# Kernel optimization log

Measured on AMD Instinct MI355X. Metric: run time of the kernel, lower is better.

The kernel has to match this reference:

```python
import jax, jax.numpy as jnp
import numpy as np

BATCH = 2048
N = 2 * BATCH
TEMP = 0.5
BN_EPS = 1e-5
COS_EPS = 1e-8

# Precompute (constant) flat indices of the negative entries: all (i,j) with
# j != i and j != i +- BATCH. Each row has exactly N-2 negatives.
_mask = np.ones((N, N), dtype=bool)
np.fill_diagonal(_mask, False)
for _i in range(BATCH):
    _mask[_i, BATCH + _i] = False
    _mask[BATCH + _i, _i] = False
NEG_IDX = np.nonzero(_mask.reshape(-1))[0]  # (N*(N-2),)


def _projector(h, W1, gamma, beta, W2, b2):
    # Linear (no bias) -> BatchNorm1d (training-mode batch stats) -> ReLU -> Linear
    x = h @ W1.T                                   # (B, latent)
    mu = jnp.mean(x, axis=0)
    var = jnp.mean(jnp.square(x - mu), axis=0)     # biased var, as torch BN
    x = (x - mu) * jax.lax.rsqrt(var + BN_EPS) * gamma + beta
    x = jax.nn.relu(x)
    return x @ W2.T + b2                           # (B, proj)


def setup_inputs() -> dict:
    key = jax.random.key(0)
    ks = jax.random.split(key, 4)
    latent, proj = 2048, 256
    return {
        "h_i": jax.random.normal(ks[0], (BATCH, latent), jnp.float32),
        "h_j": jax.random.normal(ks[1], (BATCH, latent), jnp.float32),
        "W1": jax.random.normal(ks[2], (latent, latent), jnp.float32) / np.sqrt(latent),
        "gamma": jnp.ones((latent,), jnp.float32),
        "beta": jnp.zeros((latent,), jnp.float32),
        "W2": jax.random.normal(ks[3], (proj, latent), jnp.float32) / np.sqrt(latent),
        "b2": jnp.zeros((proj,), jnp.float32),
    }


def reference(h_i, h_j, W1, gamma, beta, W2, b2):
    z_i = _projector(h_i, W1, gamma, beta, W2, b2)
    z_j = _projector(h_j, W1, gamma, beta, W2, b2)
    z = jnp.concatenate([z_i, z_j], axis=0)                      # (N, proj)
    # cosine similarity: normalize once, then a single GEMM
    zn = z / jnp.maximum(jnp.linalg.norm(z, axis=1, keepdims=True), COS_EPS)
    sim = (zn @ zn.T) / TEMP                                     # (N, N)
    sim_i_j = jnp.diagonal(sim, offset=BATCH)                    # (BATCH,)
    sim_j_i = jnp.diagonal(sim, offset=-BATCH)                   # (BATCH,)
    positives = jnp.concatenate([sim_i_j, sim_j_i])[:, None]     # (N, 1)
    negatives = sim.reshape(-1)[NEG_IDX].reshape(N, N - 2)       # (N, N-2)
    logits = jnp.concatenate([positives, negatives], axis=1)     # (N, N-1)
    # cross-entropy with label 0 for every row, reduction='sum', then / N
    loss = jnp.sum(jax.nn.logsumexp(logits, axis=1) - logits[:, 0]) / N
    return loss
```

## Files before the change

### kernel.cpp

```cpp
#include <hip/hip_runtime.h>
#include <hip/hip_fp8.h>
#include <math.h>

#define BATCH   2048
#define NROWS   4096
#define LATENT  2048
#define PROJ    256
#define BN_EPS  1e-5f
#define COS_EPS 1e-8f
#define W1SCALE 32.0f
#define W1INV   (1.0f / 32.0f)
#define ZNSCALE 16.0f
#define SIMSCALE (1.0f / 128.0f)

typedef float f32x4 __attribute__((ext_vector_type(4)));
typedef long  i64;

__device__ __forceinline__ unsigned short f2bf(float f) {
    union { float f; unsigned int u; } c; c.f = f;
    return (unsigned short)((c.u + 0x7FFFu + ((c.u >> 16) & 1u)) >> 16);
}
__device__ __forceinline__ float bf2f(unsigned short h) {
    union { unsigned int u; float f; } c; c.u = ((unsigned int)h) << 16;
    return c.f;
}
__device__ __forceinline__ unsigned char f2fp8(float f) {
    __hip_fp8_e4m3 t(f);
    return (unsigned char)t.__x;
}
__device__ __forceinline__ float fp82f(unsigned char b) {
    __hip_fp8_e4m3 t; t.__x = b;
    return (float)t;
}

__device__ __forceinline__ void gl_lds16(const void* g, void* l) {
    __builtin_amdgcn_global_load_lds(
        (const __attribute__((address_space(1))) void*)g,
        (__attribute__((address_space(3))) void*)l, 16, 0, 0);
}

__device__ __forceinline__ int mix8(int R) {
    return (R & 7) ^ ((R >> 1) & 4);
}

#define G1 1048576
#define G2 2097152
#define G3 3145728
#define G4 3276800
__global__ __launch_bounds__(256) void cvt_all_kernel(
    const float* __restrict__ h_i, const float* __restrict__ h_j,
    const float* __restrict__ W1,  const float* __restrict__ W2,
    unsigned char* __restrict__ Hq, unsigned char* __restrict__ W1q,
    unsigned char* __restrict__ W2q, float* __restrict__ zeroacc)
{
    int i = blockIdx.x * 256 + threadIdx.x;
    if (blockIdx.x == 0) {
        #pragma unroll
        for (int u = 0; u < 48; ++u) zeroacc[u * 256 + threadIdx.x] = 0.f;
    }
    if (i >= G4) return;
    if (i < G2) {
        const float* src = (i < G1) ? h_i : h_j;
        int off = (i < G1) ? i : i - G1;
        float4 v = reinterpret_cast<const float4*>(src)[off];
        uchar4 o;
        o.x = f2fp8(v.x); o.y = f2fp8(v.y); o.z = f2fp8(v.z); o.w = f2fp8(v.w);
        reinterpret_cast<uchar4*>(Hq)[i] = o;
    } else if (i < G3) {
        int off = i - G2;
        float4 v = reinterpret_cast<const float4*>(W1)[off];
        uchar4 o;
        o.x = f2fp8(v.x * W1SCALE); o.y = f2fp8(v.y * W1SCALE);
        o.z = f2fp8(v.z * W1SCALE); o.w = f2fp8(v.w * W1SCALE);
        reinterpret_cast<uchar4*>(W1q)[off] = o;
    } else {
        int off = i - G3;
        float4 v = reinterpret_cast<const float4*>(W2)[off];
        uchar4 o;
        o.x = f2fp8(v.x * W1SCALE); o.y = f2fp8(v.y * W1SCALE);
        o.z = f2fp8(v.z * W1SCALE); o.w = f2fp8(v.w * W1SCALE);
        reinterpret_cast<uchar4*>(W2q)[off] = o;
    }
}

template<int KSTRIDE, int KLEN>
__device__ __forceinline__ void fp8_loop(
    const unsigned char* __restrict__ Ab, const unsigned char* __restrict__ Bb,
    unsigned char* As, unsigned char* Bs, f32x4 acc[4][2], int tid)
{
    const int wid = tid >> 6, lane = tid & 63;
    const int mblk = (wid >> 1) * 64, nblk = (wid & 1) * 32;
    const int lr = lane & 15, lk = lane >> 4;
    for (int k0 = 0; k0 < KLEN; k0 += 128) {
        __syncthreads();
        #pragma unroll
        for (int u = 0; u < 4; ++u) {
            int li = u * 256 + tid;
            int r = li >> 3, s = li & 7;
            gl_lds16(Ab + (size_t)r * KSTRIDE + k0 + ((s ^ mix8(r)) * 16), As + li * 16);
        }
        #pragma unroll
        for (int u = 0; u < 2; ++u) {
            int li = u * 256 + tid;
            int r = li >> 3, s = li & 7;
            gl_lds16(Bb + (size_t)r * KSTRIDE + k0 + ((s ^ mix8(r)) * 16), Bs + li * 16);
        }
        __syncthreads();
        i64 af[4][4], bv[2][4];
        #pragma unroll
        for (int i = 0; i < 4; ++i) {
            int R = mblk + i * 16 + lr;
            int mr = mix8(R);
            int base = R * 128 + (lk & 1) * 8;
            #pragma unroll
            for (int t = 0; t < 4; ++t) {
                int g = 2 * t + (lk >> 1);
                af[i][t] = *reinterpret_cast<const i64*>(As + base + ((g ^ mr) << 4));
            }
        }
        #pragma unroll
        for (int j = 0; j < 2; ++j) {
            int R = nblk + j * 16 + lr;
            int mr = mix8(R);
            int base = R * 128 + (lk & 1) * 8;
            #pragma unroll
            for (int t = 0; t < 4; ++t) {
                int g = 2 * t + (lk >> 1);
                bv[j][t] = *reinterpret_cast<const i64*>(Bs + base + ((g ^ mr) << 4));
            }
        }
        #pragma unroll
        for (int t = 0; t < 4; ++t)
            #pragma unroll
            for (int i = 0; i < 4; ++i)
                #pragma unroll
                for (int j = 0; j < 2; ++j)
                    acc[i][j] = __builtin_amdgcn_mfma_f32_16x16x32_fp8_fp8(
                        af[i][t], bv[j][t], acc[i][j], 0, 0, 0);
    }
}

__global__ __launch_bounds__(256, 4) void gemm1_fp8(
    const unsigned char* __restrict__ Hq, const unsigned char* __restrict__ W1q,
    unsigned char* __restrict__ Xq, float* __restrict__ sums, float* __restrict__ sumsqs)
{
    __shared__ __align__(16) unsigned char As[128 * 128];
    __shared__ __align__(16) unsigned char Bs[64 * 128];
    const int tid = threadIdx.x;
    const int m0 = blockIdx.y * 128, n0 = blockIdx.x * 64;
    f32x4 zero = {0.f, 0.f, 0.f, 0.f};
    f32x4 acc[4][2];
    #pragma unroll
    for (int i = 0; i < 4; ++i) { acc[i][0] = zero; acc[i][1] = zero; }
    fp8_loop<LATENT, LATENT>(Hq + (size_t)m0 * LATENT, W1q + (size_t)n0 * LATENT,
                             As, Bs, acc, tid);
    const int wid = tid >> 6, lane = tid & 63;
    const int mblk = (wid >> 1) * 64, nblk = (wid & 1) * 32;
    const int lr = lane & 15, lq = lane >> 4;
    const int half = m0 >> 11;
    #pragma unroll
    for (int j = 0; j < 2; ++j) {
        float s = 0.f, q = 0.f;
        #pragma unroll
        for (int i = 0; i < 4; ++i)
            #pragma unroll
            for (int r = 0; r < 4; ++r) {
                float v = acc[i][j][r] * W1INV;
                s += v; q += v * v;
                int row = m0 + mblk + i * 16 + lq * 4 + r;
                int col = n0 + nblk + j * 16 + lr;
                Xq[(size_t)row * LATENT + col] = f2fp8(v);
            }
        s += __shfl_xor(s, 16, 64);  q += __shfl_xor(q, 16, 64);
        s += __shfl_xor(s, 32, 64);  q += __shfl_xor(q, 32, 64);
        if (lq == 0) {
            int col = n0 + nblk + j * 16 + lr;
            atomicAdd(&sums[half * LATENT + col], s);
            atomicAdd(&sumsqs[half * LATENT + col], q);
        }
    }
}

__global__ __launch_bounds__(256) void bnrelu8_kernel(
    unsigned char* __restrict__ Xq, const float* __restrict__ sums,
    const float* __restrict__ sumsqs, const float* __restrict__ gamma,
    const float* __restrict__ beta)
{
    const int row = blockIdx.x;
    const int half = row >> 11;
    const int col = threadIdx.x * 8;
    size_t idx = (size_t)row * LATENT + col;
    uchar4 a = *reinterpret_cast<const uchar4*>(Xq + idx);
    uchar4 b = *reinterpret_cast<const uchar4*>(Xq + idx + 4);
    uchar4 oa, ob;
    #pragma unroll
    for (int u = 0; u < 8; ++u) {
        int c = col + u;
        int g = half * LATENT + c;
        float mu  = sums[g] * (1.0f / BATCH);
        float var = sumsqs[g] * (1.0f / BATCH) - mu * mu;
        float sc = gamma[c] * rsqrtf(var + BN_EPS);
        float sh = beta[c] - mu * sc;
        unsigned char x = (u < 4) ? ((const unsigned char*)&a)[u] : ((const unsigned char*)&b)[u - 4];
        unsigned char o = f2fp8(fmaxf(fmaf(fp82f(x), sc, sh), 0.f));
        if (u < 4) ((unsigned char*)&oa)[u] = o; else ((unsigned char*)&ob)[u - 4] = o;
    }
    *reinterpret_cast<uchar4*>(Xq + idx) = oa;
    *reinterpret_cast<uchar4*>(Xq + idx + 4) = ob;
}

__global__ __launch_bounds__(256, 4) void gemm2_fp8(
    const unsigned char* __restrict__ Xq, const unsigned char* __restrict__ W2q,
    unsigned short* __restrict__ Zpb)
{
    __shared__ __align__(16) unsigned char As[128 * 128];
    __shared__ __align__(16) unsigned char Bs[64 * 128];
    const int tid = threadIdx.x;
    const int m0 = blockIdx.y * 128, n0 = blockIdx.x * 64, kc = blockIdx.z;
    f32x4 zero = {0.f, 0.f, 0.f, 0.f};
    f32x4 acc[4][2];
    #pragma unroll
    for (int i = 0; i < 4; ++i) { acc[i][0] = zero; acc[i][1] = zero; }
    fp8_loop<LATENT, 512>(Xq + (size_t)m0 * LATENT + kc * 512,
                          W2q + (size_t)n0 * LATENT + kc * 512, As, Bs, acc, tid);
    unsigned short* Zk = Zpb + (size_t)kc * NROWS * PROJ;
    const int wid = tid >> 6, lane = tid & 63;
    const int mblk = (wid >> 1) * 64, nblk = (wid & 1) * 32;
    const int lr = lane & 15, lq = lane >> 4;
    #pragma unroll
    for (int i = 0; i < 4; ++i)
        #pragma unroll
        for (int j = 0; j < 2; ++j)
            #pragma unroll
            for (int r = 0; r < 4; ++r) {
                int row = m0 + mblk + i * 16 + lq * 4 + r;
                int col = n0 + nblk + j * 16 + lr;
                Zk[(size_t)row * PROJ + col] = f2bf(acc[i][j][r] * W1INV);
            }
}

__global__ __launch_bounds__(256) void rownorm_kernel(
    const unsigned short* __restrict__ Zpb, const float* __restrict__ b2,
    unsigned char* __restrict__ ZNq)
{
    const int wave = threadIdx.x >> 6;
    const int lane = threadIdx.x & 63;
    const int row = blockIdx.x * 4 + wave;
    float v[4];
    float sq = 0.f;
    #pragma unroll
    for (int i = 0; i < 4; ++i) {
        int col = lane + i * 64;
        float t = b2[col];
        #pragma unroll
        for (int c = 0; c < 4; ++c)
            t += bf2f(Zpb[(size_t)c * NROWS * PROJ + (size_t)row * PROJ + col]);
        v[i] = t;
        sq += t * t;
    }
    #pragma unroll
    for (int off = 32; off > 0; off >>= 1) sq += __shfl_xor(sq, off, 64);
    float inv = ZNSCALE / fmaxf(sqrtf(sq), COS_EPS);
    #pragma unroll
    for (int i = 0; i < 4; ++i)
        ZNq[(size_t)row * PROJ + lane + i * 64] = f2fp8(v[i] * inv);
}

__global__ __launch_bounds__(256) void simlse_fp8(
    const unsigned char* __restrict__ ZNq, float* __restrict__ rowsum,
    float* __restrict__ dgA, float* __restrict__ posA)
{
    if (blockIdx.x < blockIdx.y) return;
    __shared__ __align__(16) unsigned char As[128 * 256];
    __shared__ __align__(16) unsigned char Bs[128 * 256];
    const int tid = threadIdx.x;
    const int r0 = blockIdx.y * 128, j0 = blockIdx.x * 128;
    const bool offdiag = (j0 != r0);
    const unsigned char* Ab = ZNq + (size_t)r0 * PROJ;
    const unsigned char* Bb = ZNq + (size_t)j0 * PROJ;
    #pragma unroll
    for (int u = 0; u < 8; ++u) {
        int li = u * 256 + tid;
        int r = li >> 4, s = li & 15;
        int c = s ^ (r & 15);
        gl_lds16(Ab + (size_t)r * PROJ + c * 16, As + li * 16);
    }
    #pragma unroll
    for (int u = 0; u < 8; ++u) {
        int li = u * 256 + tid;
        int r = li >> 4, s = li & 15;
        int c = s ^ (r & 15);
        gl_lds16(Bb + (size_t)r * PROJ + c * 16, Bs + li * 16);
    }
    __syncthreads();
    const int wid = tid >> 6, lane = tid & 63;
    const int mblk = (wid >> 1) * 64, nblk = (wid & 1) * 64;
    const int lr = lane & 15, lk = lane >> 4;
    f32x4 zero = {0.f, 0.f, 0.f, 0.f};
    f32x4 acc[4][4];
    #pragma unroll
    for (int i = 0; i < 4; ++i)
        #pragma unroll
        for (int j = 0; j < 4; ++j) acc[i][j] = zero;
    #pragma unroll
    for (int t = 0; t < 8; ++t) {
        int g = 2 * t + (lk >> 1);
        i64 af[4], bv[4];
        #pragma unroll
        for (int i = 0; i < 4; ++i) {
            int R = mblk + i * 16 + lr;
            af[i] = *reinterpret_cast<const i64*>(As + R * 256 + ((g ^ (R & 15)) << 4) + (lk & 1) * 8);
        }
        #pragma unroll
        for (int j = 0; j < 4; ++j) {
            int R = nblk + j * 16 + lr;
            bv[j] = *reinterpret_cast<const i64*>(Bs + R * 256 + ((g ^ (R & 15)) << 4) + (lk & 1) * 8);
        }
        #pragma unroll
        for (int i = 0; i < 4; ++i)
            #pragma unroll
            for (int j = 0; j < 4; ++j)
                acc[i][j] = __builtin_amdgcn_mfma_f32_16x16x32_fp8_fp8(af[i], bv[j], acc[i][j], 0, 0, 0);
    }
    const int lq = lane >> 4;
    float tcol[4] = {0.f, 0.f, 0.f, 0.f};
    #pragma unroll
    for (int i = 0; i < 4; ++i)
        #pragma unroll
        for (int r = 0; r < 4; ++r) {
            int R = r0 + mblk + i * 16 + lq * 4 + r;
            int P = (R < BATCH) ? R + BATCH : R - BATCH;
            float t = 0.f;
            #pragma unroll
            for (int j = 0; j < 4; ++j) {
                int J = j0 + nblk + j * 16 + lr;
                float s = acc[i][j][r] * SIMSCALE;
                float e = __expf(s);
                t += e;
                tcol[j] += e;
                if (J == R) dgA[R] = e;
                if (J == P) { posA[R] = s; posA[J] = s; }
            }
            t += __shfl_xor(t, 1, 64);
            t += __shfl_xor(t, 2, 64);
            t += __shfl_xor(t, 4, 64);
            t += __shfl_xor(t, 8, 64);
            if (lr == 0) atomicAdd(&rowsum[R], t);
        }
    if (offdiag) {
        #pragma unroll
        for (int j = 0; j < 4; ++j) {
            float c = tcol[j];
            c += __shfl_xor(c, 16, 64);
            c += __shfl_xor(c, 32, 64);
            if (lq == 0) atomicAdd(&rowsum[j0 + nblk + j * 16 + lr], c);
        }
    }
}

__global__ __launch_bounds__(256) void loss_kernel(
    const float* __restrict__ rowsum, const float* __restrict__ dgA,
    const float* __restrict__ posA, float* __restrict__ out)
{
    __shared__ float red[256];
    float s = 0.f;
    for (int r = threadIdx.x; r < NROWS; r += 256)
        s += logf(rowsum[r] - dgA[r]) - posA[r];
    red[threadIdx.x] = s;
    __syncthreads();
    for (int off = 128; off > 0; off >>= 1) {
        if (threadIdx.x < off) red[threadIdx.x] += red[threadIdx.x + off];
        __syncthreads();
    }
    if (threadIdx.x == 0) out[0] = red[0] * (1.0f / NROWS);
}

extern "C" void kernel_launch(void* const* d_in, const int* in_sizes, int n_in,
                              void* d_out, int out_size, void* d_ws, size_t ws_size,
                              hipStream_t stream)
{
    const float* h_i   = (const float*)d_in[0];
    const float* h_j   = (const float*)d_in[1];
    const float* W1    = (const float*)d_in[2];
    const float* gamma = (const float*)d_in[3];
    const float* beta  = (const float*)d_in[4];
    const float* W2    = (const float*)d_in[5];
    const float* b2    = (const float*)d_in[6];
    float* out = (float*)d_out;

    unsigned short* Zpb = (unsigned short*)d_ws;
    float* sums   = (float*)(Zpb + (size_t)4 * NROWS * PROJ);
    float* sumsqs = sums + 2 * LATENT;
    float* rowsum = sumsqs + 2 * LATENT;
    float* dgA    = rowsum + NROWS;
    float* posA   = dgA + NROWS;
    unsigned char* Hq  = (unsigned char*)(posA + NROWS);
    unsigned char* W1q = Hq + (size_t)NROWS * LATENT;
    unsigned char* W2q = W1q + (size_t)LATENT * LATENT;
    unsigned char* Xq  = W2q + (size_t)PROJ * LATENT;
    unsigned char* ZNq = Xq + (size_t)NROWS * LATENT;

    cvt_all_kernel<<<(G4 + 255) / 256, 256, 0, stream>>>(h_i, h_j, W1, W2, Hq, W1q, W2q, sums);
    gemm1_fp8<<<dim3(LATENT / 64, NROWS / 128), 256, 0, stream>>>(Hq, W1q, Xq, sums, sumsqs);
    bnrelu8_kernel<<<NROWS, 256, 0, stream>>>(Xq, sums, sumsqs, gamma, beta);
    gemm2_fp8<<<dim3(PROJ / 64, NROWS / 128, 4), 256, 0, stream>>>(Xq, W2q, Zpb);
    rownorm_kernel<<<NROWS / 4, 256, 0, stream>>>(Zpb, b2, ZNq);
    simlse_fp8<<<dim3(NROWS / 128, NROWS / 128), 256, 0, stream>>>(ZNq, rowsum, dgA, posA);
    loss_kernel<<<1, 256, 0, stream>>>(rowsum, dgA, posA, out);
}
```

Baseline: 173.3 us.

## Fuse second projection GEMM with row normalization into single kernel

Replaces the split-K gemm2 (which wrote four bf16 partial Z buffers) and the separate rownorm kernel with one kernel. Each block computes a full 128x256 output tile over the whole K dimension, adds the bias, reduces squared norms across the two column waves through shared memory, and writes normalized fp8 rows directly. This removes the partial-sum round trip through global memory and one launch. The cost is only 32 blocks for this GEMM, which leaves most CUs idle, plus more accumulator registers per thread (acc[4][8]).

```diff
diff --git a/kernel.cpp b/kernel.cpp
--- a/kernel.cpp
+++ b/kernel.cpp
@@ -16,14 +16,6 @@
 typedef float f32x4 __attribute__((ext_vector_type(4)));
 typedef long  i64;
 
-__device__ __forceinline__ unsigned short f2bf(float f) {
-    union { float f; unsigned int u; } c; c.f = f;
-    return (unsigned short)((c.u + 0x7FFFu + ((c.u >> 16) & 1u)) >> 16);
-}
-__device__ __forceinline__ float bf2f(unsigned short h) {
-    union { unsigned int u; float f; } c; c.u = ((unsigned int)h) << 16;
-    return c.f;
-}
 __device__ __forceinline__ unsigned char f2fp8(float f) {
     __hip_fp8_e4m3 t(f);
     return (unsigned char)t.__x;
@@ -32,13 +24,11 @@
     __hip_fp8_e4m3 t; t.__x = b;
     return (float)t;
 }
-
 __device__ __forceinline__ void gl_lds16(const void* g, void* l) {
     __builtin_amdgcn_global_load_lds(
         (const __attribute__((address_space(1))) void*)g,
         (__attribute__((address_space(3))) void*)l, 16, 0, 0);
 }
-
 __device__ __forceinline__ int mix8(int R) {
     return (R & 7) ^ ((R >> 1) & 4);
 }
@@ -209,61 +199,98 @@
     *reinterpret_cast<uchar4*>(Xq + idx + 4) = ob;
 }
 
-__global__ __launch_bounds__(256, 4) void gemm2_fp8(
+__global__ __launch_bounds__(256) void gemm2rn_fp8(
     const unsigned char* __restrict__ Xq, const unsigned char* __restrict__ W2q,
-    unsigned short* __restrict__ Zpb)
+    const float* __restrict__ b2, unsigned char* __restrict__ ZNq)
 {
     __shared__ __align__(16) unsigned char As[128 * 128];
-    __shared__ __align__(16) unsigned char Bs[64 * 128];
+    __shared__ __align__(16) unsigned char Bs[256 * 128];
+    __shared__ float red[128][2];
     const int tid = threadIdx.x;
-    const int m0 = blockIdx.y * 128, n0 = blockIdx.x * 64, kc = blockIdx.z;
+    const int m0 = blockIdx.x * 128;
+    const unsigned char* Ab = Xq + (size_t)m0 * LATENT;
+    const int wid = tid >> 6, lane = tid & 63;
+    const int mblk = (wid >> 1) * 64, nblk = (wid & 1) * 128;
+    const int lr = lane & 15, lk = lane >> 4;
     f32x4 zero = {0.f, 0.f, 0.f, 0.f};
-    f32x4 acc[4][2];
-    #pragma unroll
-    for (int i = 0; i < 4; ++i) { acc[i][0] = zero; acc[i][1] = zero; }
-    fp8_loop<LATENT, 512>(Xq + (size_t)m0 * LATENT + kc * 512,
-                          W2q + (size_t)n0 * LATENT + kc * 512, As, Bs, acc, tid);
-    unsigned short* Zk = Zpb + (size_t)kc * NROWS * PROJ;
-    const int wid = tid >> 6, lane = tid & 63;
-    const int mblk = (wid >> 1) * 64, nblk = (wid & 1) * 32;
-    const int lr = lane & 15, lq = lane >> 4;
+    f32x4 acc[4][8];
     #pragma unroll
     for (int i = 0; i < 4; ++i)
         #pragma unroll
-        for (int j = 0; j < 2; ++j)
-            #pragma unroll
-            for (int r = 0; r < 4; ++r) {
-                int row = m0 + mblk + i * 16 + lq * 4 + r;
-                int col = n0 + nblk + j * 16 + lr;
-                Zk[(size_t)row * PROJ + col] = f2bf(acc[i][j][r] * W1INV);
-            }
-}
-
-__global__ __launch_bounds__(256) void rownorm_kernel(
-    const unsigned short* __restrict__ Zpb, const float* __restrict__ b2,
-    unsigned char* __restrict__ ZNq)
-{
-    const int wave = threadIdx.x >> 6;
-    const int lane = threadIdx.x & 63;
-    const int row = blockIdx.x * 4 + wave;
-    float v[4];
-    float sq = 0.f;
-    #pragma unroll
-    for (int i = 0; i < 4; ++i) {
-        int col = lane + i * 64;
-        float t = b2[col];
-        #pragma unroll
-        for (int c = 0; c < 4; ++c)
-            t += bf2f(Zpb[(size_t)c * NROWS * PROJ + (size_t)row * PROJ + col]);
-        v[i] = t;
-        sq += t * t;
-    }
-    #pragma unroll
-    for (int off = 32; off > 0; off >>= 1) sq += __shfl_xor(sq, off, 64);
-    float inv = ZNSCALE / fmaxf(sqrtf(sq), COS_EPS);
+        for (int j = 0; j < 8; ++j) acc[i][j] = zero;
+
+    for (int k0 = 0; k0 < LATENT; k0 += 128) {
+        __syncthreads();
+        #pragma unroll
+        for (int u = 0; u < 4; ++u) {
+            int li = u * 256 + tid;
+            int r = li >> 3, s = li & 7;
+            gl_lds16(Ab + (size_t)r * LATENT + k0 + ((s ^ mix8(r)) * 16), As + li * 16);
+        }
+        #pragma unroll
+        for (int u = 0; u < 8; ++u) {
+            int li = u * 256 + tid;
+            int r = li >> 3, s = li & 7;
+            gl_lds16(W2q + (size_t)r * LATENT + k0 + ((s ^ mix8(r)) * 16), Bs + li * 16);
+        }
+        __syncthreads();
+        #pragma unroll
+        for (int t = 0; t < 4; ++t) {
+            int g = 2 * t + (lk >> 1);
+            i64 af[4], bv[8];
+            #pragma unroll
+            for (int i = 0; i < 4; ++i) {
+                int R = mblk + i * 16 + lr;
+                af[i] = *reinterpret_cast<const i64*>(As + R * 128 + ((g ^ mix8(R)) << 4) + (lk & 1) * 8);
+            }
+            #pragma unroll
+            for (int j = 0; j < 8; ++j) {
+                int R = nblk + j * 16 + lr;
+                bv[j] = *reinterpret_cast<const i64*>(Bs + R * 128 + ((g ^ mix8(R)) << 4) + (lk & 1) * 8);
+            }
+            #pragma unroll
+            for (int i = 0; i < 4; ++i)
+                #pragma unroll
+                for (int j = 0; j < 8; ++j)
+                    acc[i][j] = __builtin_amdgcn_mfma_f32_16x16x32_fp8_fp8(af[i], bv[j], acc[i][j], 0, 0, 0);
+        }
+    }
+
+    const int lq = lane >> 4;
+    float b2v[8];
+    #pragma unroll
+    for (int j = 0; j < 8; ++j) b2v[j] = b2[nblk + j * 16 + lr];
     #pragma unroll
     for (int i = 0; i < 4; ++i)
-        ZNq[(size_t)row * PROJ + lane + i * 64] = f2fp8(v[i] * inv);
+        #pragma unroll
+        for (int r = 0; r < 4; ++r) {
+            float sq = 0.f;
+            #pragma unroll
+            for (int j = 0; j < 8; ++j) {
+                float z = fmaf(acc[i][j][r], W1INV, b2v[j]);
+                sq += z * z;
+            }
+            sq += __shfl_xor(sq, 1, 64);
+            sq += __shfl_xor(sq, 2, 64);
+            sq += __shfl_xor(sq, 4, 64);
+            sq += __shfl_xor(sq, 8, 64);
+            if (lr == 0) red[mblk + i * 16 + lq * 4 + r][wid & 1] = sq;
+        }
+    __syncthreads();
+    #pragma unroll
+    for (int i = 0; i < 4; ++i)
+        #pragma unroll
+        for (int r = 0; r < 4; ++r) {
+            int rl = mblk + i * 16 + lq * 4 + r;
+            float sq = red[rl][0] + red[rl][1];
+            float inv = ZNSCALE / fmaxf(sqrtf(sq), COS_EPS);
+            size_t rowbase = (size_t)(m0 + rl) * PROJ;
+            #pragma unroll
+            for (int j = 0; j < 8; ++j) {
+                float z = fmaf(acc[i][j][r], W1INV, b2v[j]);
+                ZNq[rowbase + nblk + j * 16 + lr] = f2fp8(z * inv);
+            }
+        }
 }
 
 __global__ __launch_bounds__(256) void simlse_fp8(
@@ -282,15 +309,13 @@
     for (int u = 0; u < 8; ++u) {
         int li = u * 256 + tid;
         int r = li >> 4, s = li & 15;
-        int c = s ^ (r & 15);
-        gl_lds16(Ab + (size_t)r * PROJ + c * 16, As + li * 16);
+        gl_lds16(Ab + (size_t)r * PROJ + ((s ^ (r & 15)) * 16), As + li * 16);
     }
     #pragma unroll
     for (int u = 0; u < 8; ++u) {
         int li = u * 256 + tid;
         int r = li >> 4, s = li & 15;
-        int c = s ^ (r & 15);
-        gl_lds16(Bb + (size_t)r * PROJ + c * 16, Bs + li * 16);
+        gl_lds16(Bb + (size_t)r * PROJ + ((s ^ (r & 15)) * 16), Bs + li * 16);
     }
     __syncthreads();
     const int wid = tid >> 6, lane = tid & 63;
@@ -388,8 +413,7 @@
     const float* b2    = (const float*)d_in[6];
     float* out = (float*)d_out;
 
-    unsigned short* Zpb = (unsigned short*)d_ws;
-    float* sums   = (float*)(Zpb + (size_t)4 * NROWS * PROJ);
+    float* sums   = (float*)d_ws;
     float* sumsqs = sums + 2 * LATENT;
     float* rowsum = sumsqs + 2 * LATENT;
     float* dgA    = rowsum + NROWS;
@@ -403,8 +427,7 @@
     cvt_all_kernel<<<(G4 + 255) / 256, 256, 0, stream>>>(h_i, h_j, W1, W2, Hq, W1q, W2q, sums);
     gemm1_fp8<<<dim3(LATENT / 64, NROWS / 128), 256, 0, stream>>>(Hq, W1q, Xq, sums, sumsqs);
     bnrelu8_kernel<<<NROWS, 256, 0, stream>>>(Xq, sums, sumsqs, gamma, beta);
-    gemm2_fp8<<<dim3(PROJ / 64, NROWS / 128, 4), 256, 0, stream>>>(Xq, W2q, Zpb);
-    rownorm_kernel<<<NROWS / 4, 256, 0, stream>>>(Zpb, b2, ZNq);
+    gemm2rn_fp8<<<NROWS / 128, 256, 0, stream>>>(Xq, W2q, b2, ZNq);
     simlse_fp8<<<dim3(NROWS / 128, NROWS / 128), 256, 0, stream>>>(ZNq, rowsum, dgA, posA);
     loss_kernel<<<1, 256, 0, stream>>>(rowsum, dgA, posA, out);
 }
```

Result: slower. 202.3 us (+16.8%).

## Fuse rownorm into gemm2 and loss into simlse via last-block atomic counters

Applied to the files above, without the earlier changes.

Removes two kernel launches by having the last-arriving block of each gemm2 row tile (tracked with an atomic counter) perform the bias add, row normalization and fp8 quantization, and the last simlse block perform the final loss reduction. Split-K partials are now stored as fp32 instead of bf16 to avoid conversions, which doubles the partial-buffer traffic. Counters are zeroed in the conversion kernel by extending its zero-fill. The row normalization now runs serially in only 32 winner blocks, which may lengthen the tail, and the workspace layout changes.

```diff
diff --git a/kernel.cpp b/kernel.cpp
--- a/kernel.cpp
+++ b/kernel.cpp
@@ -16,14 +16,6 @@
 typedef float f32x4 __attribute__((ext_vector_type(4)));
 typedef long  i64;
 
-__device__ __forceinline__ unsigned short f2bf(float f) {
-    union { float f; unsigned int u; } c; c.f = f;
-    return (unsigned short)((c.u + 0x7FFFu + ((c.u >> 16) & 1u)) >> 16);
-}
-__device__ __forceinline__ float bf2f(unsigned short h) {
-    union { unsigned int u; float f; } c; c.u = ((unsigned int)h) << 16;
-    return c.f;
-}
 __device__ __forceinline__ unsigned char f2fp8(float f) {
     __hip_fp8_e4m3 t(f);
     return (unsigned char)t.__x;
@@ -32,15 +24,16 @@
     __hip_fp8_e4m3 t; t.__x = b;
     return (float)t;
 }
-
 __device__ __forceinline__ void gl_lds16(const void* g, void* l) {
     __builtin_amdgcn_global_load_lds(
         (const __attribute__((address_space(1))) void*)g,
         (__attribute__((address_space(3))) void*)l, 16, 0, 0);
 }
-
 __device__ __forceinline__ int mix8(int R) {
     return (R & 7) ^ ((R >> 1) & 4);
+}
+__device__ __forceinline__ float aload(const float* p) {
+    return __hip_atomic_load(p, __ATOMIC_RELAXED, __HIP_MEMORY_SCOPE_AGENT);
 }
 
 #define G1 1048576
@@ -56,7 +49,7 @@
     int i = blockIdx.x * 256 + threadIdx.x;
     if (blockIdx.x == 0) {
         #pragma unroll
-        for (int u = 0; u < 48; ++u) zeroacc[u * 256 + threadIdx.x] = 0.f;
+        for (int u = 0; u < 49; ++u) zeroacc[u * 256 + threadIdx.x] = 0.f;
     }
     if (i >= G4) return;
     if (i < G2) {
@@ -209,12 +202,14 @@
     *reinterpret_cast<uchar4*>(Xq + idx + 4) = ob;
 }
 
-__global__ __launch_bounds__(256, 4) void gemm2_fp8(
+__global__ __launch_bounds__(256) void gemm2_fp8(
     const unsigned char* __restrict__ Xq, const unsigned char* __restrict__ W2q,
-    unsigned short* __restrict__ Zpb)
+    float* __restrict__ Zp, const float* __restrict__ b2,
+    unsigned char* __restrict__ ZNq, int* __restrict__ cnt)
 {
     __shared__ __align__(16) unsigned char As[128 * 128];
     __shared__ __align__(16) unsigned char Bs[64 * 128];
+    __shared__ int iswin;
     const int tid = threadIdx.x;
     const int m0 = blockIdx.y * 128, n0 = blockIdx.x * 64, kc = blockIdx.z;
     f32x4 zero = {0.f, 0.f, 0.f, 0.f};
@@ -223,7 +218,7 @@
     for (int i = 0; i < 4; ++i) { acc[i][0] = zero; acc[i][1] = zero; }
     fp8_loop<LATENT, 512>(Xq + (size_t)m0 * LATENT + kc * 512,
                           W2q + (size_t)n0 * LATENT + kc * 512, As, Bs, acc, tid);
-    unsigned short* Zk = Zpb + (size_t)kc * NROWS * PROJ;
+    float* Zk = Zp + (size_t)kc * NROWS * PROJ;
     const int wid = tid >> 6, lane = tid & 63;
     const int mblk = (wid >> 1) * 64, nblk = (wid & 1) * 32;
     const int lr = lane & 15, lq = lane >> 4;
@@ -235,44 +230,49 @@
             for (int r = 0; r < 4; ++r) {
                 int row = m0 + mblk + i * 16 + lq * 4 + r;
                 int col = n0 + nblk + j * 16 + lr;
-                Zk[(size_t)row * PROJ + col] = f2bf(acc[i][j][r] * W1INV);
+                Zk[(size_t)row * PROJ + col] = acc[i][j][r] * W1INV;
             }
-}
-
-__global__ __launch_bounds__(256) void rownorm_kernel(
-    const unsigned short* __restrict__ Zpb, const float* __restrict__ b2,
-    unsigned char* __restrict__ ZNq)
-{
-    const int wave = threadIdx.x >> 6;
-    const int lane = threadIdx.x & 63;
-    const int row = blockIdx.x * 4 + wave;
-    float v[4];
-    float sq = 0.f;
-    #pragma unroll
-    for (int i = 0; i < 4; ++i) {
-        int col = lane + i * 64;
-        float t = b2[col];
-        #pragma unroll
-        for (int c = 0; c < 4; ++c)
-            t += bf2f(Zpb[(size_t)c * NROWS * PROJ + (size_t)row * PROJ + col]);
-        v[i] = t;
-        sq += t * t;
-    }
-    #pragma unroll
-    for (int off = 32; off > 0; off >>= 1) sq += __shfl_xor(sq, off, 64);
-    float inv = ZNSCALE / fmaxf(sqrtf(sq), COS_EPS);
-    #pragma unroll
-    for (int i = 0; i < 4; ++i)
-        ZNq[(size_t)row * PROJ + lane + i * 64] = f2fp8(v[i] * inv);
+    __threadfence();
+    if (tid == 0) {
+        int old = atomicAdd(&cnt[blockIdx.y], 1);
+        iswin = (old == 15);
+    }
+    __syncthreads();
+    if (!iswin) return;
+    __threadfence();
+    const int wave = tid >> 6, ln = tid & 63;
+    for (int rr = wave; rr < 128; rr += 4) {
+        int row = m0 + rr;
+        float v[4];
+        float sq = 0.f;
+        #pragma unroll
+        for (int i = 0; i < 4; ++i) {
+            int col = ln + i * 64;
+            float t = b2[col];
+            #pragma unroll
+            for (int c = 0; c < 4; ++c)
+                t += aload(&Zp[(size_t)c * NROWS * PROJ + (size_t)row * PROJ + col]);
+            v[i] = t;
+            sq += t * t;
+        }
+        #pragma unroll
+        for (int off = 32; off > 0; off >>= 1) sq += __shfl_xor(sq, off, 64);
+        float inv = ZNSCALE / fmaxf(sqrtf(sq), COS_EPS);
+        #pragma unroll
+        for (int i = 0; i < 4; ++i)
+            ZNq[(size_t)row * PROJ + ln + i * 64] = f2fp8(v[i] * inv);
+    }
 }
 
 __global__ __launch_bounds__(256) void simlse_fp8(
     const unsigned char* __restrict__ ZNq, float* __restrict__ rowsum,
-    float* __restrict__ dgA, float* __restrict__ posA)
+    float* __restrict__ dgA, float* __restrict__ posA,
+    int* __restrict__ cnt, float* __restrict__ out)
 {
     if (blockIdx.x < blockIdx.y) return;
     __shared__ __align__(16) unsigned char As[128 * 256];
     __shared__ __align__(16) unsigned char Bs[128 * 256];
+    __shared__ int iswin;
     const int tid = threadIdx.x;
     const int r0 = blockIdx.y * 128, j0 = blockIdx.x * 128;
     const bool offdiag = (j0 != r0);
@@ -282,15 +282,13 @@
     for (int u = 0; u < 8; ++u) {
         int li = u * 256 + tid;
         int r = li >> 4, s = li & 15;
-        int c = s ^ (r & 15);
-        gl_lds16(Ab + (size_t)r * PROJ + c * 16, As + li * 16);
+        gl_lds16(Ab + (size_t)r * PROJ + ((s ^ (r & 15)) * 16), As + li * 16);
     }
     #pragma unroll
     for (int u = 0; u < 8; ++u) {
         int li = u * 256 + tid;
         int r = li >> 4, s = li & 15;
-        int c = s ^ (r & 15);
-        gl_lds16(Bb + (size_t)r * PROJ + c * 16, Bs + li * 16);
+        gl_lds16(Bb + (size_t)r * PROJ + ((s ^ (r & 15)) * 16), Bs + li * 16);
     }
     __syncthreads();
     const int wid = tid >> 6, lane = tid & 63;
@@ -356,23 +354,25 @@
             if (lq == 0) atomicAdd(&rowsum[j0 + nblk + j * 16 + lr], c);
         }
     }
-}
-
-__global__ __launch_bounds__(256) void loss_kernel(
-    const float* __restrict__ rowsum, const float* __restrict__ dgA,
-    const float* __restrict__ posA, float* __restrict__ out)
-{
-    __shared__ float red[256];
+    __threadfence();
+    if (tid == 0) {
+        int old = atomicAdd(cnt, 1);
+        iswin = (old == 527);
+    }
+    __syncthreads();
+    if (!iswin) return;
+    __threadfence();
+    float* red = (float*)As;
     float s = 0.f;
-    for (int r = threadIdx.x; r < NROWS; r += 256)
-        s += logf(rowsum[r] - dgA[r]) - posA[r];
-    red[threadIdx.x] = s;
+    for (int r = tid; r < NROWS; r += 256)
+        s += logf(aload(&rowsum[r]) - aload(&dgA[r])) - aload(&posA[r]);
+    red[tid] = s;
     __syncthreads();
     for (int off = 128; off > 0; off >>= 1) {
-        if (threadIdx.x < off) red[threadIdx.x] += red[threadIdx.x + off];
+        if (tid < off) red[tid] += red[tid + off];
         __syncthreads();
     }
-    if (threadIdx.x == 0) out[0] = red[0] * (1.0f / NROWS);
+    if (tid == 0) out[0] = red[0] * (1.0f / NROWS);
 }
 
 extern "C" void kernel_launch(void* const* d_in, const int* in_sizes, int n_in,
@@ -388,13 +388,14 @@
     const float* b2    = (const float*)d_in[6];
     float* out = (float*)d_out;
 
-    unsigned short* Zpb = (unsigned short*)d_ws;
-    float* sums   = (float*)(Zpb + (size_t)4 * NROWS * PROJ);
+    float* sums   = (float*)d_ws;
     float* sumsqs = sums + 2 * LATENT;
     float* rowsum = sumsqs + 2 * LATENT;
-    float* dgA    = rowsum + NROWS;
+    int*   cnt    = (int*)(rowsum + NROWS);
+    float* dgA    = (float*)(cnt + 256);
     float* posA   = dgA + NROWS;
-    unsigned char* Hq  = (unsigned char*)(posA + NROWS);
+    float* Zp     = posA + NROWS;
+    unsigned char* Hq  = (unsigned char*)(Zp + (size_t)4 * NROWS * PROJ);
     unsigned char* W1q = Hq + (size_t)NROWS * LATENT;
     unsigned char* W2q = W1q + (size_t)LATENT * LATENT;
     unsigned char* Xq  = W2q + (size_t)PROJ * LATENT;
@@ -403,8 +404,6 @@
     cvt_all_kernel<<<(G4 + 255) / 256, 256, 0, stream>>>(h_i, h_j, W1, W2, Hq, W1q, W2q, sums);
     gemm1_fp8<<<dim3(LATENT / 64, NROWS / 128), 256, 0, stream>>>(Hq, W1q, Xq, sums, sumsqs);
     bnrelu8_kernel<<<NROWS, 256, 0, stream>>>(Xq, sums, sumsqs, gamma, beta);
-    gemm2_fp8<<<dim3(PROJ / 64, NROWS / 128, 4), 256, 0, stream>>>(Xq, W2q, Zpb);
-    rownorm_kernel<<<NROWS / 4, 256, 0, stream>>>(Zpb, b2, ZNq);
-    simlse_fp8<<<dim3(NROWS / 128, NROWS / 128), 256, 0, stream>>>(ZNq, rowsum, dgA, posA);
-    loss_kernel<<<1, 256, 0, stream>>>(rowsum, dgA, posA, out);
-}
+    gemm2_fp8<<<dim3(PROJ / 64, NROWS / 128, 4), 256, 0, stream>>>(Xq, W2q, Zp, b2, ZNq, cnt);
+    simlse_fp8<<<dim3(NROWS / 128, NROWS / 128), 256, 0, stream>>>(ZNq, rowsum, dgA, posA, cnt + 32, out);
+}
```

New measurement: 291.5 us. +68.2%, slower.
